# Kernel tuning notes

Measured on AMD Instinct MI355X. Metric: run time of the kernel, lower is better.

The kernel has to match this reference:

```python
import jax, jax.numpy as jnp
import numpy as np

B, T, C = 4, 2048, 1024
H, DH = 16, 64  # num_heads, head_size; H*DH == C


def setup_inputs() -> dict:
    key = jax.random.key(0)
    ks = jax.random.split(key, 6)
    s = C ** -0.5
    x = jax.random.normal(ks[0], (B, T, C), dtype=jnp.float32)
    # per-head projection weights, stacked: [H, C, DH]
    Wq = jax.random.normal(ks[1], (H, C, DH), dtype=jnp.float32) * s
    Wk = jax.random.normal(ks[2], (H, C, DH), dtype=jnp.float32) * s
    Wv = jax.random.normal(ks[3], (H, C, DH), dtype=jnp.float32) * s
    # output projection (with bias, as nn.Linear default)
    Wo = jax.random.normal(ks[4], (C, C), dtype=jnp.float32) * s
    bo = jax.random.normal(ks[5], (C,), dtype=jnp.float32) * 0.01
    return {"x": x, "Wq": Wq, "Wk": Wk, "Wv": Wv, "Wo": Wo, "bo": bo}


def reference(x, Wq, Wk, Wv, Wo, bo):
    Bv, Tv, Cv = x.shape
    scale = DH ** -0.5
    # project to per-head q/k/v: [B, H, T, DH]
    q = jnp.einsum('btc,hcd->bhtd', x, Wq)
    k = jnp.einsum('btc,hcd->bhtd', x, Wk)
    v = jnp.einsum('btc,hcd->bhtd', x, Wv)
    # scaled scores [B, H, T, T] with causal mask
    scores = jnp.einsum('bhtd,bhsd->bhts', q, k) * scale
    causal = jnp.tril(jnp.ones((Tv, Tv), dtype=bool))
    scores = jnp.where(causal, scores, -jnp.inf)
    wei = jax.nn.softmax(scores, axis=-1)
    out = jnp.einsum('bhts,bhsd->bhtd', wei, v)
    # concat heads: [B, T, H*DH] == [B, T, C]
    out = out.transpose(0, 2, 1, 3).reshape(Bv, Tv, Cv)
    return out @ Wo.T + bo
```

## Files before the change

### kernel.cpp

```cpp
#include <hip/hip_runtime.h>
#include <stdint.h>

typedef unsigned short u16;
typedef __attribute__((ext_vector_type(8))) short short8;
typedef __attribute__((ext_vector_type(4))) float floatx4;

#define MFMA_BF16 __builtin_amdgcn_mfma_f32_16x16x32_bf16

#define BB 4
#define TT 2048
#define CC 1024
#define HH 16
#define DH 64
#define MM (BB * TT)
#define NQKV (3 * CC)

__device__ __forceinline__ u16 f2bf(float f) {
  union { float f; uint32_t u; } un;
  un.f = f;
  uint32_t u = un.u;
  u += 0x7fffu + ((u >> 16) & 1u);
  return (u16)(u >> 16);
}

__device__ __forceinline__ uint32_t pk2(float a, float b) {
  return (uint32_t)f2bf(a) | ((uint32_t)f2bf(b) << 16);
}

__device__ __forceinline__ uint32_t pktrunc(float a, float b) {
  union { float f; uint32_t u; } ua, ub;
  ua.f = a; ub.f = b;
  return __builtin_amdgcn_perm(ub.u, ua.u, 0x07060302u);
}

__device__ __forceinline__ void gload_lds16(const u16* g, u16* l) {
  __builtin_amdgcn_global_load_lds(
      (const __attribute__((address_space(1))) unsigned int*)g,
      (__attribute__((address_space(3))) unsigned int*)l, 16, 0, 0);
}

__device__ __forceinline__ void BAR() {
  asm volatile("" ::: "memory");
  __builtin_amdgcn_s_barrier();
  asm volatile("" ::: "memory");
}

__global__ __launch_bounds__(256) void convert_kernel(
    const float* __restrict__ x, const float* __restrict__ Wq,
    const float* __restrict__ Wk, const float* __restrict__ Wv,
    const float* __restrict__ Wo, u16* __restrict__ xb,
    u16* __restrict__ Wt, u16* __restrict__ Wob) {
  __shared__ float T[32][33];
  int bid = blockIdx.x, tid = threadIdx.x;
  if (bid < 8192) {
    int i = (bid * 256 + tid) * 4;
    float4 f = *(const float4*)(x + i);
    uint2 o = {pk2(f.x, f.y), pk2(f.z, f.w)};
    *(uint2*)(xb + i) = o;
  } else if (bid < 8192 + 3072) {
    int tb = bid - 8192;
    int sec = tb >> 10, rem = tb & 1023;
    int h = rem >> 6, sub = rem & 63, ct = sub >> 1, dt = sub & 1;
    const float* W = (sec == 0) ? Wq : (sec == 1) ? Wk : Wv;
    int tx = tid & 31, ty = tid >> 5;
#pragma unroll
    for (int p = 0; p < 4; ++p)
      T[ty + 8 * p][tx] =
          W[((size_t)h * CC + ct * 32 + ty + 8 * p) * DH + dt * 32 + tx];
    __syncthreads();
#pragma unroll
    for (int p = 0; p < 4; ++p) {
      int n = sec * 1024 + h * 64 + dt * 32 + ty + 8 * p;
      Wt[(size_t)n * CC + ct * 32 + tx] = f2bf(T[tx][ty + 8 * p]);
    }
  } else {
    int i = ((bid - 11264) * 256 + tid) * 4;
    float4 f = *(const float4*)(Wo + i);
    uint2 o = {pk2(f.x, f.y), pk2(f.z, f.w)};
    *(uint2*)(Wob + i) = o;
  }
}

__global__ __launch_bounds__(512, 2) void gemm_qkv(
    const u16* __restrict__ A, const u16* __restrict__ Bt,
    u16* __restrict__ qout, u16* __restrict__ kout, u16* __restrict__ vout) {
  __shared__ u16 As[3 * 128 * 32];
  __shared__ u16 Bs[3 * 384 * 32];

  int tid = threadIdx.x;
  int lane = tid & 63, w = tid >> 6;
  int wr = w >> 2, wc = w & 3;
  int g = lane >> 4, c = lane & 15;
  int m0 = blockIdx.y * 128, n0 = blockIdx.x * 384;

  floatx4 acc[4][6];
#pragma unroll
  for (int i = 0; i < 4; ++i)
#pragma unroll
    for (int j = 0; j < 6; ++j) acc[i][j] = (floatx4){0.f, 0.f, 0.f, 0.f};

  int arow = tid >> 2, acol = (tid & 3) * 8;
  const u16* Ag = A + (size_t)(m0 + arow) * CC + acol;
  const u16* Bg = Bt + (size_t)(n0 + arow) * CC + acol;
  u16* asd = As + tid * 8;
  u16* bsd = Bs + tid * 8;

  int aro = (wr * 64 + c) * 32 + g * 8;
  int bro = (wc * 96 + c) * 32 + g * 8;

  gload_lds16(Ag, asd);
  gload_lds16(Bg, bsd);
  gload_lds16(Bg + (size_t)128 * CC, bsd + 4096);
  gload_lds16(Bg + (size_t)256 * CC, bsd + 8192);
  gload_lds16(Ag + 32, asd + 4096);
  gload_lds16(Bg + 32, bsd + 12288);
  gload_lds16(Bg + 32 + (size_t)128 * CC, bsd + 12288 + 4096);
  gload_lds16(Bg + 32 + (size_t)256 * CC, bsd + 12288 + 8192);
  asm volatile("s_waitcnt vmcnt(4)" ::: "memory");
  BAR();

#define QTILE(SCA, SCB, SPA, SPB, T2, STG, VMW)                               \
  {                                                                           \
    short8 af0 = *(const short8*)(As + (SCA) + aro);                          \
    short8 af1 = *(const short8*)(As + (SCA) + aro + 512);                    \
    short8 af2 = *(const short8*)(As + (SCA) + aro + 1024);                   \
    short8 af3 = *(const short8*)(As + (SCA) + aro + 1536);                   \
    short8 bv0 = *(const short8*)(Bs + (SCB) + bro);                          \
    short8 bv1 = *(const short8*)(Bs + (SCB) + bro + 512);                    \
    short8 bv2 = *(const short8*)(Bs + (SCB) + bro + 1024);                   \
    if (STG) {                                                                \
      gload_lds16(Ag + (size_t)(T2) * 32, asd + (SPA));                       \
      gload_lds16(Bg + (size_t)(T2) * 32, bsd + (SPB));                       \
    }                                                                         \
    BAR();                                                                    \
    __builtin_amdgcn_s_setprio(1);                                            \
    acc[0][0] = MFMA_BF16(af0, bv0, acc[0][0], 0, 0, 0);                      \
    acc[0][1] = MFMA_BF16(af0, bv1, acc[0][1], 0, 0, 0);                      \
    acc[0][2] = MFMA_BF16(af0, bv2, acc[0][2], 0, 0, 0);                      \
    acc[1][0] = MFMA_BF16(af1, bv0, acc[1][0], 0, 0, 0);                      \
    acc[1][1] = MFMA_BF16(af1, bv1, acc[1][1], 0, 0, 0);                      \
    acc[1][2] = MFMA_BF16(af1, bv2, acc[1][2], 0, 0, 0);                      \
    acc[2][0] = MFMA_BF16(af2, bv0, acc[2][0], 0, 0, 0);                      \
    acc[2][1] = MFMA_BF16(af2, bv1, acc[2][1], 0, 0, 0);                      \
    acc[2][2] = MFMA_BF16(af2, bv2, acc[2][2], 0, 0, 0);                      \
    acc[3][0] = MFMA_BF16(af3, bv0, acc[3][0], 0, 0, 0);                      \
    acc[3][1] = MFMA_BF16(af3, bv1, acc[3][1], 0, 0, 0);                      \
    acc[3][2] = MFMA_BF16(af3, bv2, acc[3][2], 0, 0, 0);                      \
    __builtin_amdgcn_s_setprio(0);                                            \
    BAR();                                                                    \
    short8 bv3 = *(const short8*)(Bs + (SCB) + bro + 1536);                   \
    short8 bv4 = *(const short8*)(Bs + (SCB) + bro + 2048);                   \
    short8 bv5 = *(const short8*)(Bs + (SCB) + bro + 2560);                   \
    if (STG) {                                                                \
      gload_lds16(Bg + (size_t)(T2) * 32 + (size_t)128 * CC,                  \
                  bsd + (SPB) + 4096);                                        \
      gload_lds16(Bg + (size_t)(T2) * 32 + (size_t)256 * CC,                  \
                  bsd + (SPB) + 8192);                                        \
    }                                                                         \
    BAR();                                                                    \
    __builtin_amdgcn_s_setprio(1);                                            \
    acc[0][3] = MFMA_BF16(af0, bv3, acc[0][3], 0, 0, 0);                      \
    acc[0][4] = MFMA_BF16(af0, bv4, acc[0][4], 0, 0, 0);                      \
    acc[0][5] = MFMA_BF16(af0, bv5, acc[0][5], 0, 0, 0);                      \
    acc[1][3] = MFMA_BF16(af1, bv3, acc[1][3], 0, 0, 0);                      \
    acc[1][4] = MFMA_BF16(af1, bv4, acc[1][4], 0, 0, 0);                      \
    acc[1][5] = MFMA_BF16(af1, bv5, acc[1][5], 0, 0, 0);                      \
    acc[2][3] = MFMA_BF16(af2, bv3, acc[2][3], 0, 0, 0);                      \
    acc[2][4] = MFMA_BF16(af2, bv4, acc[2][4], 0, 0, 0);                      \
    acc[2][5] = MFMA_BF16(af2, bv5, acc[2][5], 0, 0, 0);                      \
    acc[3][3] = MFMA_BF16(af3, bv3, acc[3][3], 0, 0, 0);                      \
    acc[3][4] = MFMA_BF16(af3, bv4, acc[3][4], 0, 0, 0);                      \
    acc[3][5] = MFMA_BF16(af3, bv5, acc[3][5], 0, 0, 0);                      \
    __builtin_amdgcn_s_setprio(0);                                            \
    VMW;                                                                      \
    BAR();                                                                    \
  }

  int scA = 0, snA = 4096, spA = 8192;
  int scB = 0, snB = 12288, spB = 24576;
#pragma unroll 1
  for (int t = 0; t < 30; ++t) {
    QTILE(scA, scB, spA, spB, t + 2, 1,
          asm volatile("s_waitcnt vmcnt(4)" ::: "memory"));
    int ta = scA; scA = snA; snA = spA; spA = ta;
    int tb = scB; scB = snB; snB = spB; spB = tb;
  }
  QTILE(scA, scB, spA, spB, 0, 0,
        asm volatile("s_waitcnt vmcnt(0)" ::: "memory"));
  {
    int ta = scA; scA = snA; snA = spA; spA = ta;
    int tb = scB; scB = snB; snB = spB; spB = tb;
  }
  QTILE(scA, scB, spA, spB, 0, 0, (void)0);
#undef QTILE

  int mrow = m0 + wr * 64 + g * 4;
  int ncol = n0 + wc * 96 + c;
#pragma unroll
  for (int nt = 0; nt < 6; ++nt) {
    int n = ncol + nt * 16;
    int sec = n >> 10, h = (n >> 6) & 15, d = n & 63;
    u16* dst = (sec == 0) ? qout : (sec == 1) ? kout : vout;
    float sc = (sec == 0) ? 0.18033688011112042f : 1.f;
#pragma unroll
    for (int mt = 0; mt < 4; ++mt) {
#pragma unroll
      for (int r = 0; r < 4; ++r) {
        int m = mrow + mt * 16 + r;
        int b = m >> 11, t = m & 2047;
        dst[(((size_t)(b * HH + h)) * TT + t) * DH + d] =
            f2bf(acc[mt][nt][r] * sc);
      }
    }
  }
}

template <int MODE>
__global__ __launch_bounds__(256) void gemm_bt(
    const u16* __restrict__ A, const u16* __restrict__ Bt, int M, int N, int K,
    u16* __restrict__ qout, u16* __restrict__ kout, u16* __restrict__ vout,
    float* __restrict__ out, const float* __restrict__ bias) {
  __shared__ u16 As[128][64];
  __shared__ u16 Bs[128][64];
  int tid = threadIdx.x;
  int lane = tid & 63, w = tid >> 6;
  int wm = w >> 1, wn = w & 1;
  int g = lane >> 4, c = lane & 15;
  int m0 = blockIdx.y * 128, n0 = blockIdx.x * 128;

  floatx4 acc[4][4];
#pragma unroll
  for (int i = 0; i < 4; ++i)
#pragma unroll
    for (int j = 0; j < 4; ++j) acc[i][j] = (floatx4){0.f, 0.f, 0.f, 0.f};

  int srow = 32 * w + (lane >> 3);
  int scol = (lane & 7) * 8;
  const u16* Ag = A + (size_t)(m0 + srow) * K + scol;
  const u16* Bg = Bt + (size_t)(n0 + srow) * K + scol;
  u16* AsB = &As[32 * w][0];
  u16* BsB = &Bs[32 * w][0];

  for (int k0 = 0; k0 < K; k0 += 64) {
    __syncthreads();
#pragma unroll
    for (int j = 0; j < 4; ++j)
      gload_lds16(Ag + k0 + (size_t)j * 8 * K, AsB + j * 512);
#pragma unroll
    for (int j = 0; j < 4; ++j)
      gload_lds16(Bg + k0 + (size_t)j * 8 * K, BsB + j * 512);
    __syncthreads();
#pragma unroll
    for (int kc = 0; kc < 2; ++kc) {
      short8 af[4], bfv[4];
#pragma unroll
      for (int mt = 0; mt < 4; ++mt)
        af[mt] = *(const short8*)(&As[wm * 64 + mt * 16 + c][kc * 32 + g * 8]);
#pragma unroll
      for (int nt = 0; nt < 4; ++nt)
        bfv[nt] = *(const short8*)(&Bs[wn * 64 + nt * 16 + c][kc * 32 + g * 8]);
#pragma unroll
      for (int mt = 0; mt < 4; ++mt)
#pragma unroll
        for (int nt = 0; nt < 4; ++nt)
          acc[mt][nt] = MFMA_BF16(af[mt], bfv[nt], acc[mt][nt], 0, 0, 0);
    }
  }

#pragma unroll
  for (int mt = 0; mt < 4; ++mt) {
#pragma unroll
    for (int nt = 0; nt < 4; ++nt) {
#pragma unroll
      for (int r = 0; r < 4; ++r) {
        int m = m0 + wm * 64 + mt * 16 + g * 4 + r;
        int n = n0 + wn * 64 + nt * 16 + c;
        float v = acc[mt][nt][r];
        if (MODE == 0) {
          int b = m >> 11, t = m & 2047;
          int sec = n >> 10, h = (n >> 6) & 15, d = n & 63;
          size_t idx = (((size_t)(b * HH + h)) * TT + t) * DH + d;
          if (sec == 0)
            qout[idx] = f2bf(v * 0.18033688011112042f);
          else if (sec == 1)
            kout[idx] = f2bf(v);
          else
            vout[idx] = f2bf(v);
        } else {
          out[(size_t)m * N + n] = v + bias[n];
        }
      }
    }
  }
}

__global__ __launch_bounds__(256) void vtrans(const u16* __restrict__ v,
                                              u16* __restrict__ vP) {
  __shared__ u16 Ld[64][72];
  int tile = blockIdx.x, bh = blockIdx.y, tid = threadIdx.x;
  int row = tid >> 2, col = (tid & 3) * 16;
  const u16* src = v + ((size_t)bh * TT + tile * 64 + row) * DH + col;
  *(uint4*)(&Ld[row][col]) = *(const uint4*)(src);
  *(uint4*)(&Ld[row][col + 8]) = *(const uint4*)(src + 8);
  __syncthreads();
  int d = tid >> 2, u0 = (tid & 3) * 16;
  union { u16 h[16]; uint4 q[2]; } o;
#pragma unroll
  for (int k = 0; k < 16; ++k) {
    int u = u0 + k;
    int s = ((u & 3) << 4) | (u >> 2);
    o.h[k] = Ld[s][d];
  }
  u16* dst = vP + ((size_t)(bh * DH + d)) * TT + tile * 64 + u0;
  *(uint4*)(dst) = o.q[0];
  *(uint4*)(dst + 8) = o.q[1];
}

__constant__ unsigned char CHUNK_X[24] = {15, 15, 7, 14, 14, 13, 13, 6,
                                          12, 12, 11, 11, 5, 10, 10, 9,
                                          9,  4,  8,  8,  3, 2,  1,  0};
__constant__ unsigned char CHUNK_H[24] = {0, 1, 2, 0, 1, 0, 1, 2, 0, 1, 0, 1,
                                          2, 0, 1, 0, 1, 2, 0, 1, 2, 2, 2, 2};

__global__ __launch_bounds__(256, 4) void flash_attn(
    const u16* __restrict__ q, const u16* __restrict__ k,
    const u16* __restrict__ vP, u16* __restrict__ O,
    float* __restrict__ opart, float* __restrict__ lpart) {
  __shared__ u16 Ks[64][72];
  __shared__ u16 Vs[64][72];
  __shared__ u16 Ps[4][32][72];

  int tid = threadIdx.x;
  int lane = tid & 63, w = tid >> 6;
  int g = lane >> 4, c = lane & 15;

  int id = blockIdx.x;
  int e = id >> 6, bh = id & 63;
  int x = CHUNK_X[e], hf = CHUNK_H[e];
  int sb, se;
  if (hf == 2) {
    sb = 0; se = 2 * x + 2;
  } else {
    int n = x + 1; sb = hf * n; se = sb + n;
  }
  int t0 = x << 7;

  const u16* qb = q + (size_t)bh * TT * DH;
  const u16* kb = k + (size_t)bh * TT * DH;
  const u16* vb = vP + (size_t)bh * DH * TT;

  short8 qf[2][2];
#pragma unroll
  for (int mt = 0; mt < 2; ++mt) {
    int qrow = t0 + w * 32 + mt * 16 + c;
#pragma unroll
    for (int kc = 0; kc < 2; ++kc)
      qf[mt][kc] = *(const short8*)(qb + (size_t)qrow * DH + kc * 32 + g * 8);
  }

  const floatx4 zf = {0.f, 0.f, 0.f, 0.f};
  const short8 onesf = {(short)0x3F80, (short)0x3F80, (short)0x3F80,
                        (short)0x3F80, (short)0x3F80, (short)0x3F80,
                        (short)0x3F80, (short)0x3F80};

  floatx4 oacc[2][4];
#pragma unroll
  for (int mt = 0; mt < 2; ++mt)
#pragma unroll
    for (int nt = 0; nt < 4; ++nt) oacc[mt][nt] = zf;
  floatx4 lacc[2];
  lacc[0] = zf;
  lacc[1] = zf;

  int srow = tid >> 2, scol = (tid & 3) * 16;
  const u16* kbase = kb + (size_t)srow * DH + scol;
  const u16* vbase = vb + (size_t)srow * TT + scol;

  uint4 kr0 = *(const uint4*)(kbase + (size_t)(sb << 6) * DH);
  uint4 kr1 = *(const uint4*)(kbase + (size_t)(sb << 6) * DH + 8);
  uint4 vr0 = *(const uint4*)(vbase + (sb << 6));
  uint4 vr1 = *(const uint4*)(vbase + (sb << 6) + 8);

  int nfull = 2 * x;
  int wmax = t0 + w * 32 + 31;
  for (int it = sb; it < se; ++it) {
    int s0 = it << 6;
    __syncthreads();
    *(uint4*)(&Ks[srow][scol]) = kr0;
    *(uint4*)(&Ks[srow][scol + 8]) = kr1;
    *(uint4*)(&Vs[srow][scol]) = vr0;
    *(uint4*)(&Vs[srow][scol + 8]) = vr1;
    __syncthreads();
    if (it + 1 < se) {
      size_t koff = (size_t)((it + 1) << 6) * DH;
      int voff = (it + 1) << 6;
      kr0 = *(const uint4*)(kbase + koff);
      kr1 = *(const uint4*)(kbase + koff + 8);
      vr0 = *(const uint4*)(vbase + voff);
      vr1 = *(const uint4*)(vbase + voff + 8);
    }
    if (s0 > wmax) continue;
    bool masked = (it >= nfull);

    floatx4 z[2][4];
#pragma unroll
    for (int n = 0; n < 4; ++n) {
      short8 kf = *(const short8*)(&Ks[n * 16 + c][g * 8]);
      z[0][n] = MFMA_BF16(qf[0][0], kf, zf, 0, 0, 0);
      z[1][n] = MFMA_BF16(qf[1][0], kf, zf, 0, 0, 0);
    }
#pragma unroll
    for (int n = 0; n < 4; ++n) {
      short8 kf = *(const short8*)(&Ks[n * 16 + c][32 + g * 8]);
      z[0][n] = MFMA_BF16(qf[0][1], kf, z[0][n], 0, 0, 0);
      z[1][n] = MFMA_BF16(qf[1][1], kf, z[1][n], 0, 0, 0);
    }

#pragma unroll
    for (int mt = 0; mt < 2; ++mt) {
      int qr = t0 + w * 32 + mt * 16 + g * 4;
#pragma unroll
      for (int r = 0; r < 4; ++r) {
        float p0 = exp2f(z[mt][0][r]);
        float p1 = exp2f(z[mt][1][r]);
        float p2 = exp2f(z[mt][2][r]);
        float p3 = exp2f(z[mt][3][r]);
        if (masked) {
          if (s0 + c > qr + r) p0 = 0.f;
          if (s0 + 16 + c > qr + r) p1 = 0.f;
          if (s0 + 32 + c > qr + r) p2 = 0.f;
          if (s0 + 48 + c > qr + r) p3 = 0.f;
        }
        uint2 pk = {pktrunc(p0, p1), pktrunc(p2, p3)};
        *(uint2*)(&Ps[w][mt * 16 + g * 4 + r][4 * c]) = pk;
      }
    }

#pragma unroll
    for (int kc = 0; kc < 2; ++kc) {
      short8 pf0 = *(const short8*)(&Ps[w][c][kc * 32 + g * 8]);
      short8 pf1 = *(const short8*)(&Ps[w][16 + c][kc * 32 + g * 8]);
      lacc[0] = MFMA_BF16(pf0, onesf, lacc[0], 0, 0, 0);
      lacc[1] = MFMA_BF16(pf1, onesf, lacc[1], 0, 0, 0);
#pragma unroll
      for (int nt = 0; nt < 4; ++nt) {
        short8 vf = *(const short8*)(&Vs[nt * 16 + c][kc * 32 + g * 8]);
        oacc[0][nt] = MFMA_BF16(pf0, vf, oacc[0][nt], 0, 0, 0);
        oacc[1][nt] = MFMA_BF16(pf1, vf, oacc[1][nt], 0, 0, 0);
      }
    }
  }

  int b = bh >> 4, h = bh & 15;
  if (hf == 2) {
#pragma unroll
    for (int mt = 0; mt < 2; ++mt) {
      float inv[4];
#pragma unroll
      for (int r = 0; r < 4; ++r) inv[r] = 1.f / lacc[mt][r];
#pragma unroll
      for (int nt = 0; nt < 4; ++nt)
#pragma unroll
        for (int r = 0; r < 4; ++r) {
          int trow = t0 + w * 32 + mt * 16 + g * 4 + r;
          O[((size_t)b * TT + trow) * CC + h * DH + nt * 16 + c] =
              f2bf(oacc[mt][nt][r] * inv[r]);
        }
    }
  } else {
    float* os = opart + ((size_t)hf * 65536 + (size_t)bh * 1024) * 64;
    float* ls = lpart + (size_t)hf * 65536 + (size_t)bh * 1024;
#pragma unroll
    for (int mt = 0; mt < 2; ++mt) {
      int r0 = t0 - 1024 + w * 32 + mt * 16 + g * 4;
#pragma unroll
      for (int nt = 0; nt < 4; ++nt)
#pragma unroll
        for (int r = 0; r < 4; ++r)
          os[(size_t)(r0 + r) * 64 + nt * 16 + c] = oacc[mt][nt][r];
      if (c == 0)
#pragma unroll
        for (int r = 0; r < 4; ++r) ls[r0 + r] = lacc[mt][r];
    }
  }
}

__global__ __launch_bounds__(256) void merge_heavy(
    const float* __restrict__ op, const float* __restrict__ lp,
    u16* __restrict__ O) {
  int gid = blockIdx.x * 256 + threadIdx.x;
  int dq = gid & 15;
  int row = gid >> 4;
  float4 a = *(const float4*)(op + (size_t)row * 64 + dq * 4);
  float4 b = *(const float4*)(op + ((size_t)row + 65536) * 64 + dq * 4);
  float inv = 1.f / (lp[row] + lp[row + 65536]);
  int bh = row >> 10, lr = row & 1023;
  int bb = bh >> 4, h = bh & 15;
  u16* dst = O + ((size_t)bb * TT + 1024 + lr) * CC + h * DH + dq * 4;
  uint2 o = {pk2((a.x + b.x) * inv, (a.y + b.y) * inv),
             pk2((a.z + b.z) * inv, (a.w + b.w) * inv)};
  *(uint2*)dst = o;
}

extern "C" void kernel_launch(void* const* d_in, const int* in_sizes, int n_in,
                              void* d_out, int out_size, void* d_ws,
                              size_t ws_size, hipStream_t stream) {
  const float* x = (const float*)d_in[0];
  const float* Wq = (const float*)d_in[1];
  const float* Wk = (const float*)d_in[2];
  const float* Wv = (const float*)d_in[3];
  const float* Wo = (const float*)d_in[4];
  const float* bo = (const float*)d_in[5];
  float* out = (float*)d_out;

  u16* ws = (u16*)d_ws;
  u16* xb = ws;
  u16* Wt = xb + 8388608;
  u16* Wob = Wt + 3145728;
  u16* qw = Wob + 1048576;
  u16* kw = qw + 8388608;
  u16* vw = kw + 8388608;
  u16* vP = vw + 8388608;
  u16* Ow = xb;
  float* opart = (float*)d_out;
  float* lpart = (float*)Wt;

  convert_kernel<<<12288, 256, 0, stream>>>(x, Wq, Wk, Wv, Wo, xb, Wt, Wob);

  gemm_qkv<<<dim3(NQKV / 384, MM / 128), 512, 0, stream>>>(
      xb, Wt, qw, kw, vw);

  vtrans<<<dim3(TT / 64, BB * HH), 256, 0, stream>>>(vw, vP);

  flash_attn<<<dim3(1536), 256, 0, stream>>>(qw, kw, vP, Ow, opart, lpart);

  merge_heavy<<<dim3(4096), 256, 0, stream>>>(opart, lpart, Ow);

  gemm_bt<1><<<dim3(CC / 128, MM / 128), 256, 0, stream>>>(
      Ow, Wob, MM, CC, CC, nullptr, nullptr, nullptr, out, bo);
}
```

Measured before the change: 280.3 us.

## Load K/V MFMA fragments directly from global into registers, drop shared staging

Removes the shared-memory K and V tiles and the two block-wide barriers per iteration. Each wave now loads its K and V MFMA operand fragments straight from global memory into registers and prefetches the next tile's fragments right after they are consumed. Each wave's loop is also capped at its own causal limit, so waves no longer idle on tiles they would skip. In exchange, every wave redundantly loads the same K/V tiles, which raises global/L2 traffic, and the higher register count lowers the occupancy hint from 4 to 3 blocks.

Result: slower. 342.9 us (+22.3%).

```diff
diff --git a/kernel.cpp b/kernel.cpp
--- a/kernel.cpp
+++ b/kernel.cpp
@@ -322,12 +322,10 @@
 __constant__ unsigned char CHUNK_H[24] = {0, 1, 2, 0, 1, 0, 1, 2, 0, 1, 0, 1,
                                           2, 0, 1, 0, 1, 2, 0, 1, 2, 2, 2, 2};
 
-__global__ __launch_bounds__(256, 4) void flash_attn(
+__global__ __launch_bounds__(256, 3) void flash_attn(
     const u16* __restrict__ q, const u16* __restrict__ k,
     const u16* __restrict__ vP, u16* __restrict__ O,
     float* __restrict__ opart, float* __restrict__ lpart) {
-  __shared__ u16 Ks[64][72];
-  __shared__ u16 Vs[64][72];
   __shared__ u16 Ps[4][32][72];
 
   int tid = threadIdx.x;
@@ -349,6 +347,11 @@
   const u16* kb = k + (size_t)bh * TT * DH;
   const u16* vb = vP + (size_t)bh * DH * TT;
 
+  int wmax = t0 + w * 32 + 31;
+  int sewv = (wmax >> 6) + 1;
+  int sew = se < sewv ? se : sewv;
+  int nfull = 2 * x;
+
   short8 qf[2][2];
 #pragma unroll
   for (int mt = 0; mt < 2; ++mt) {
@@ -372,48 +375,39 @@
   lacc[0] = zf;
   lacc[1] = zf;
 
-  int srow = tid >> 2, scol = (tid & 3) * 16;
-  const u16* kbase = kb + (size_t)srow * DH + scol;
-  const u16* vbase = vb + (size_t)srow * TT + scol;
-
-  uint4 kr0 = *(const uint4*)(kbase + (size_t)(sb << 6) * DH);
-  uint4 kr1 = *(const uint4*)(kbase + (size_t)(sb << 6) * DH + 8);
-  uint4 vr0 = *(const uint4*)(vbase + (sb << 6));
-  uint4 vr1 = *(const uint4*)(vbase + (sb << 6) + 8);
-
-  int nfull = 2 * x;
-  int wmax = t0 + w * 32 + 31;
-  for (int it = sb; it < se; ++it) {
+  const u16* kfb = kb + (size_t)c * DH + g * 8;
+  const u16* vfb = vb + (size_t)c * TT + g * 8;
+
+  short8 kf[8], vf[8];
+  {
+    int s0 = sb << 6;
+#pragma unroll
+    for (int kc = 0; kc < 2; ++kc)
+#pragma unroll
+      for (int n = 0; n < 4; ++n) {
+        kf[kc * 4 + n] =
+            *(const short8*)(kfb + (size_t)(s0 + n * 16) * DH + kc * 32);
+        vf[kc * 4 + n] =
+            *(const short8*)(vfb + (size_t)(n * 16) * TT + s0 + kc * 32);
+      }
+  }
+
+  for (int it = sb; it < sew; ++it) {
     int s0 = it << 6;
-    __syncthreads();
-    *(uint4*)(&Ks[srow][scol]) = kr0;
-    *(uint4*)(&Ks[srow][scol + 8]) = kr1;
-    *(uint4*)(&Vs[srow][scol]) = vr0;
-    *(uint4*)(&Vs[srow][scol + 8]) = vr1;
-    __syncthreads();
-    if (it + 1 < se) {
-      size_t koff = (size_t)((it + 1) << 6) * DH;
-      int voff = (it + 1) << 6;
-      kr0 = *(const uint4*)(kbase + koff);
-      kr1 = *(const uint4*)(kbase + koff + 8);
-      vr0 = *(const uint4*)(vbase + voff);
-      vr1 = *(const uint4*)(vbase + voff + 8);
-    }
-    if (s0 > wmax) continue;
     bool masked = (it >= nfull);
-
-    floatx4 z[2][4];
+    int itn = (it + 1 < sew) ? it + 1 : it;
+    int s1 = itn << 6;
+
+    floatx4 z0[4], z1[4];
 #pragma unroll
     for (int n = 0; n < 4; ++n) {
-      short8 kf = *(const short8*)(&Ks[n * 16 + c][g * 8]);
-      z[0][n] = MFMA_BF16(qf[0][0], kf, zf, 0, 0, 0);
-      z[1][n] = MFMA_BF16(qf[1][0], kf, zf, 0, 0, 0);
+      z0[n] = MFMA_BF16(qf[0][0], kf[n], zf, 0, 0, 0);
+      z1[n] = MFMA_BF16(qf[1][0], kf[n], zf, 0, 0, 0);
     }
 #pragma unroll
     for (int n = 0; n < 4; ++n) {
-      short8 kf = *(const short8*)(&Ks[n * 16 + c][32 + g * 8]);
-      z[0][n] = MFMA_BF16(qf[0][1], kf, z[0][n], 0, 0, 0);
-      z[1][n] = MFMA_BF16(qf[1][1], kf, z[1][n], 0, 0, 0);
+      z0[n] = MFMA_BF16(qf[0][1], kf[4 + n], z0[n], 0, 0, 0);
+      z1[n] = MFMA_BF16(qf[1][1], kf[4 + n], z1[n], 0, 0, 0);
     }
 
 #pragma unroll
@@ -421,10 +415,10 @@
       int qr = t0 + w * 32 + mt * 16 + g * 4;
 #pragma unroll
       for (int r = 0; r < 4; ++r) {
-        float p0 = exp2f(z[mt][0][r]);
-        float p1 = exp2f(z[mt][1][r]);
-        float p2 = exp2f(z[mt][2][r]);
-        float p3 = exp2f(z[mt][3][r]);
+        float p0 = exp2f((mt ? z1 : z0)[0][r]);
+        float p1 = exp2f((mt ? z1 : z0)[1][r]);
+        float p2 = exp2f((mt ? z1 : z0)[2][r]);
+        float p3 = exp2f((mt ? z1 : z0)[3][r]);
         if (masked) {
           if (s0 + c > qr + r) p0 = 0.f;
           if (s0 + 16 + c > qr + r) p1 = 0.f;
@@ -437,6 +431,13 @@
     }
 
 #pragma unroll
+    for (int kc = 0; kc < 2; ++kc)
+#pragma unroll
+      for (int n = 0; n < 4; ++n)
+        kf[kc * 4 + n] =
+            *(const short8*)(kfb + (size_t)(s1 + n * 16) * DH + kc * 32);
+
+#pragma unroll
     for (int kc = 0; kc < 2; ++kc) {
       short8 pf0 = *(const short8*)(&Ps[w][c][kc * 32 + g * 8]);
       short8 pf1 = *(const short8*)(&Ps[w][16 + c][kc * 32 + g * 8]);
@@ -444,11 +445,17 @@
       lacc[1] = MFMA_BF16(pf1, onesf, lacc[1], 0, 0, 0);
 #pragma unroll
       for (int nt = 0; nt < 4; ++nt) {
-        short8 vf = *(const short8*)(&Vs[nt * 16 + c][kc * 32 + g * 8]);
-        oacc[0][nt] = MFMA_BF16(pf0, vf, oacc[0][nt], 0, 0, 0);
-        oacc[1][nt] = MFMA_BF16(pf1, vf, oacc[1][nt], 0, 0, 0);
+        oacc[0][nt] = MFMA_BF16(pf0, vf[kc * 4 + nt], oacc[0][nt], 0, 0, 0);
+        oacc[1][nt] = MFMA_BF16(pf1, vf[kc * 4 + nt], oacc[1][nt], 0, 0, 0);
       }
     }
+
+#pragma unroll
+    for (int kc = 0; kc < 2; ++kc)
+#pragma unroll
+      for (int nt = 0; nt < 4; ++nt)
+        vf[kc * 4 + nt] =
+            *(const short8*)(vfb + (size_t)(nt * 16) * TT + s1 + kc * 32);
   }
 
   int b = bh >> 4, h = bh & 15;
```
